# Kernel optimization log

Measured on AMD Instinct MI355X. Metric: run time of the kernel, lower is better.

Reference implementation:

```python
import jax, jax.numpy as jnp
import numpy as np

N_SUB, N_AGR, N_URB = 100000, 200000, 100000
E_SS, E_AS, E_US = 1_600_000, 400_000, 200_000
D_SUB, D_HRU, H, OUT, L = 128, 32, 128, 16, 3


def setup_inputs() -> dict:
    key = jax.random.key(0)
    ks = jax.random.split(key, 20)
    s = 0.05
    inp = {
        "x_sub": jax.random.normal(ks[0], (N_SUB, D_SUB), jnp.float32),
        "x_agr": jax.random.normal(ks[1], (N_AGR, D_HRU), jnp.float32),
        "x_urb": jax.random.normal(ks[2], (N_URB, D_HRU), jnp.float32),
        "ss_src": jax.random.randint(ks[3], (E_SS,), 0, N_SUB, jnp.int32),
        "ss_dst": jax.random.randint(ks[4], (E_SS,), 0, N_SUB, jnp.int32),
        "as_src": jax.random.randint(ks[5], (E_AS,), 0, N_AGR, jnp.int32),
        "as_dst": jax.random.randint(ks[6], (E_AS,), 0, N_SUB, jnp.int32),
        "us_src": jax.random.randint(ks[7], (E_US,), 0, N_URB, jnp.int32),
        "us_dst": jax.random.randint(ks[8], (E_US,), 0, N_SUB, jnp.int32),
        # Stacked per-layer SAGEConv params (in_sub == hidden, so uniform shapes).
        # lin_l (neighbor path, has bias) and lin_r (root path, no bias).
        "Wl_ss": jax.random.normal(ks[9], (L, H, H), jnp.float32) * s,
        "bl_ss": jnp.zeros((L, H), jnp.float32),
        "Wr_ss": jax.random.normal(ks[10], (L, H, H), jnp.float32) * s,
        "Wl_as": jax.random.normal(ks[11], (L, D_HRU, H), jnp.float32) * s,
        "bl_as": jnp.zeros((L, H), jnp.float32),
        "Wr_as": jax.random.normal(ks[12], (L, H, H), jnp.float32) * s,
        "Wl_us": jax.random.normal(ks[13], (L, D_HRU, H), jnp.float32) * s,
        "bl_us": jnp.zeros((L, H), jnp.float32),
        "Wr_us": jax.random.normal(ks[14], (L, H, H), jnp.float32) * s,
        "Wf": jax.random.normal(ks[15], (H, OUT), jnp.float32) * s,
        "bf": jnp.zeros((OUT,), jnp.float32),
    }
    return inp


def reference(x_sub, x_agr, x_urb, ss_src, ss_dst, as_src, as_dst, us_src,
              us_dst, Wl_ss, bl_ss, Wr_ss, Wl_as, bl_as, Wr_as, Wl_us, bl_us,
              Wr_us, Wf, bf):
    # Degree of each sub node under sub->sub edges (for mean aggr, layers>0).
    deg = jax.ops.segment_sum(jnp.ones((E_SS,), x_sub.dtype), ss_dst,
                              num_segments=N_SUB)
    deg = jnp.maximum(deg, 1.0)[:, None]  # [N_SUB,1]

    h = x_sub
    for i in range(L):
        # sub -> sub: gather + scatter-add (sum at layer 0, mean afterwards)
        agg_ss = jax.ops.segment_sum(h[ss_src], ss_dst, num_segments=N_SUB)
        if i > 0:
            agg_ss = agg_ss / deg  # PyG default aggr='mean' for layers > 0
        # hru_agr -> sub and hru_urb -> sub: sum aggregation (sage_aggr='sum')
        agg_as = jax.ops.segment_sum(x_agr[as_src], as_dst, num_segments=N_SUB)
        agg_us = jax.ops.segment_sum(x_urb[us_src], us_dst, num_segments=N_SUB)
        # SAGEConv: lin_l(aggr msgs) + lin_r(x_dst); HeteroConv aggr='sum'.
        out = (agg_ss @ Wl_ss[i] + bl_ss[i] + h @ Wr_ss[i]
               + agg_as @ Wl_as[i] + bl_as[i] + h @ Wr_as[i]
               + agg_us @ Wl_us[i] + bl_us[i] + h @ Wr_us[i])
        h = jax.nn.relu(out)  # norms are Identity; dropout in eval mode
    logits = h @ Wf + bf
    return jax.nn.softmax(logits, axis=1)
```

## Files before the change

### kernel.cpp

```cpp
#include <hip/hip_runtime.h>
#include <hip/hip_bf16.h>

#define N_SUB 100000
#define N_AGR 200000
#define N_URB 100000
#define E_SS  1600000
#define E_AS  400000
#define E_US  200000
#define E_TOT 2200000
#define HID   128
#define DHRU  32
#define NOUT  16
#define NL    3
#define SCAN_T 12500

typedef unsigned short u16;
typedef unsigned int u32;
typedef long long i64;
typedef short bf16x8 __attribute__((ext_vector_type(8)));
typedef float f32x4 __attribute__((ext_vector_type(4)));

#define FIXS 4294967296.0f
#define FIXR 2.3283064365386963e-10f

static __device__ __forceinline__ u16 f2b(float f) {
    u32 x = __float_as_uint(f);
    u32 r = (x + 0x7fffu + ((x >> 16) & 1u)) >> 16;
    return (u16)r;
}
static __device__ __forceinline__ float blo(u32 u) { return __uint_as_float(u << 16); }
static __device__ __forceinline__ float bhi(u32 u) { return __uint_as_float(u & 0xffff0000u); }
static __device__ __forceinline__ i64 fx(float v) { return (i64)(v * FIXS); }


__global__ void hist3_kernel(const int* __restrict__ ss_dst, const int* __restrict__ as_dst,
                             const int* __restrict__ us_dst, int* __restrict__ deg_ss,
                             int* __restrict__ deg_as, int* __restrict__ deg_us) {
    int i = blockIdx.x * 256 + threadIdx.x;
    if (i < E_SS) atomicAdd(&deg_ss[ss_dst[i]], 1);
    else if (i < E_SS + E_AS) atomicAdd(&deg_as[as_dst[i - E_SS]], 1);
    else if (i < E_TOT) atomicAdd(&deg_us[us_dst[i - E_SS - E_AS]], 1);
}

__global__ void scan_p1(const int* __restrict__ deg, int* __restrict__ tsum) {
    int i = blockIdx.x * 256 + threadIdx.x;
    if (i >= 3 * SCAN_T) return;
    const int4* p = (const int4*)(deg + i * 8);
    int4 a = p[0], b = p[1];
    tsum[i] = a.x + a.y + a.z + a.w + b.x + b.y + b.z + b.w;
}

__global__ void scan_p2(int* __restrict__ tsum_all) {
    __shared__ int sh[256];
    int* tsum = tsum_all + blockIdx.x * SCAN_T;
    const int tid = threadIdx.x;
    const int start = tid * 49;
    const int end = min(start + 49, SCAN_T);
    int s = 0;
    for (int i = start; i < end; ++i) s += tsum[i];
    sh[tid] = s;
    __syncthreads();
    for (int o = 1; o < 256; o <<= 1) {
        int t = (tid >= o) ? sh[tid - o] : 0;
        __syncthreads();
        sh[tid] += t;
        __syncthreads();
    }
    int off = (tid > 0) ? sh[tid - 1] : 0;
    for (int i = start; i < end; ++i) {
        int v = tsum[i];
        tsum[i] = off;
        off += v;
    }
}

__global__ void scan_p3(int* __restrict__ degcur, const int* __restrict__ tsum,
                        int* __restrict__ ro_ss, int* __restrict__ ro_as,
                        int* __restrict__ ro_us, float* __restrict__ inv_deg) {
    int i = blockIdx.x * 256 + threadIdx.x;
    if (i >= 3 * SCAN_T) return;
    int seg = i / SCAN_T, li = i - seg * SCAN_T;
    int* ro = (seg == 0) ? ro_ss : (seg == 1) ? ro_as : ro_us;
    int off = tsum[i];
#pragma unroll
    for (int j = 0; j < 8; ++j) {
        int gidx = i * 8 + j;
        int idx = li * 8 + j;
        int d = degcur[gidx];
        ro[idx] = off;
        if (seg == 0) inv_deg[idx] = 1.0f / (float)(d > 1 ? d : 1);
        degcur[gidx] = off;
        off += d;
    }
    if (li == SCAN_T - 1) ro[N_SUB] = off;
}

__global__ void fill3_kernel(const int* __restrict__ ss_src, const int* __restrict__ ss_dst,
                             const int* __restrict__ as_src, const int* __restrict__ as_dst,
                             const int* __restrict__ us_src, const int* __restrict__ us_dst,
                             int* __restrict__ cur_ss, int* __restrict__ cur_as,
                             int* __restrict__ cur_us, int* __restrict__ csr_ss,
                             int* __restrict__ csr_as, int* __restrict__ csr_us) {
    int i = blockIdx.x * 256 + threadIdx.x;
    const int* src; const int* dst; int* cur; int* csr; int e;
    if (i < E_SS)               { src = ss_src; dst = ss_dst; cur = cur_ss; csr = csr_ss; e = i; }
    else if (i < E_SS + E_AS)   { src = as_src; dst = as_dst; cur = cur_as; csr = csr_as; e = i - E_SS; }
    else if (i < E_TOT)         { src = us_src; dst = us_dst; cur = cur_us; csr = csr_us; e = i - E_SS - E_AS; }
    else return;
    int p = atomicAdd(&cur[dst[e]], 1);
    csr[p] = src[e];
}

__global__ __launch_bounds__(256)
void agg2_gather(const float* __restrict__ x_agr, const float* __restrict__ x_urb,
                 const int* __restrict__ ro_as, const int* __restrict__ csr_as,
                 const int* __restrict__ ro_us, const int* __restrict__ csr_us,
                 u16* __restrict__ agg2b, int n) {
    int node = blockIdx.x * 4 + (threadIdx.x >> 6);
    int lane = threadIdx.x & 63;
    if (node >= n) return;
    const bool is_us = lane >= 32;
    const int col = lane & 31;
    const int* ro = is_us ? ro_us : ro_as;
    const int* csr = is_us ? csr_us : csr_as;
    const float* x = is_us ? x_urb : x_agr;
    int beg = ro[node], end = ro[node + 1];
    i64 acc = 0;
    for (int p = beg; p < end; ++p) {
        acc += fx(x[(size_t)csr[p] * 32 + col]);
    }
    agg2b[(size_t)node * 64 + lane] = f2b((float)acc * FIXR);
}

__global__ void add3_kernel(const float* __restrict__ a, const float* __restrict__ b,
                            const float* __restrict__ c, float* __restrict__ o, int n) {
    int i = blockIdx.x * 256 + threadIdx.x;
    if (i < n) o[i] = a[i] + b[i] + c[i];
}

__global__ void build_bp(const float* __restrict__ Wl_ss, const float* __restrict__ Wr_ss,
                         const float* __restrict__ Wr_as, const float* __restrict__ Wr_us,
                         const float* __restrict__ Wl_as, const float* __restrict__ Wl_us,
                         u16* __restrict__ Bp) {
    int b = blockIdx.x;
    int lane = threadIdx.x;
    int lay = b / 80, rem = b % 80, s = rem / 8, c = rem % 8;
    int col = c * 16 + (lane & 15);
    u16* o = Bp + (size_t)(((lay * 80) + s * 8 + c) * 64 + lane) * 8;
#pragma unroll
    for (int j = 0; j < 8; ++j) {
        int k = s * 32 + (lane >> 4) * 8 + j;
        float v;
        if (k < 128) {
            v = Wl_ss[((size_t)lay * 128 + k) * 128 + col];
        } else if (k < 256) {
            size_t idx = ((size_t)lay * 128 + (k - 128)) * 128 + col;
            v = Wr_ss[idx] + Wr_as[idx] + Wr_us[idx];
        } else if (k < 288) {
            v = Wl_as[((size_t)lay * 32 + (k - 256)) * 128 + col];
        } else {
            v = Wl_us[((size_t)lay * 32 + (k - 288)) * 128 + col];
        }
        o[j] = f2b(v);
    }
}

__global__ void cvt_f32_bf16(const float* __restrict__ in, u16* __restrict__ o, int n4) {
    int i = blockIdx.x * 256 + threadIdx.x;
    if (i >= n4) return;
    float4 v = ((const float4*)in)[i];
    ushort4 u;
    u.x = f2b(v.x); u.y = f2b(v.y); u.z = f2b(v.z); u.w = f2b(v.w);
    ((ushort4*)o)[i] = u;
}

__global__ __launch_bounds__(256)
void agg_ss_bf16(const u16* __restrict__ h, const int* __restrict__ ro,
                 const int* __restrict__ csr, const float* __restrict__ inv_deg,
                 u16* __restrict__ out, int n, int use_mean) {
    int node = blockIdx.x * 4 + (threadIdx.x >> 6);
    if (node >= n) return;
    int lane = threadIdx.x & 63;
    int g = lane >> 4, t = lane & 15;
    int beg = ro[node], end = ro[node + 1];
    i64 acc[8] = {0, 0, 0, 0, 0, 0, 0, 0};
    int p = beg;
    for (; p + 3 < end; p += 4) {
        int s = csr[p + g];
        uint4 q = *(const uint4*)(h + (size_t)s * 128 + t * 8);
        acc[0] += fx(blo(q.x)); acc[1] += fx(bhi(q.x));
        acc[2] += fx(blo(q.y)); acc[3] += fx(bhi(q.y));
        acc[4] += fx(blo(q.z)); acc[5] += fx(bhi(q.z));
        acc[6] += fx(blo(q.w)); acc[7] += fx(bhi(q.w));
    }
    int rem = end - p;
    if (g < rem) {
        int s = csr[p + g];
        uint4 q = *(const uint4*)(h + (size_t)s * 128 + t * 8);
        acc[0] += fx(blo(q.x)); acc[1] += fx(bhi(q.x));
        acc[2] += fx(blo(q.y)); acc[3] += fx(bhi(q.y));
        acc[4] += fx(blo(q.z)); acc[5] += fx(bhi(q.z));
        acc[6] += fx(blo(q.w)); acc[7] += fx(bhi(q.w));
    }
#pragma unroll
    for (int j = 0; j < 8; ++j) {
        acc[j] += __shfl_xor(acc[j], 16, 64);
        acc[j] += __shfl_xor(acc[j], 32, 64);
    }
    if (g == 0) {
        float v[8];
        float iv = use_mean ? inv_deg[node] : 1.0f;
#pragma unroll
        for (int j = 0; j < 8; ++j) v[j] = (float)acc[j] * FIXR * iv;
        uint4 o;
        o.x = (u32)f2b(v[0]) | ((u32)f2b(v[1]) << 16);
        o.y = (u32)f2b(v[2]) | ((u32)f2b(v[3]) << 16);
        o.z = (u32)f2b(v[4]) | ((u32)f2b(v[5]) << 16);
        o.w = (u32)f2b(v[6]) | ((u32)f2b(v[7]) << 16);
        *(uint4*)(out + (size_t)node * 128 + t * 8) = o;
    }
}

__global__ __launch_bounds__(256)
void layer_gemm_mfma(const u16* __restrict__ agss, const u16* __restrict__ h,
                     const u16* __restrict__ agg2b, const u16* __restrict__ Bp,
                     const float* __restrict__ bsum, u16* __restrict__ out, int n) {
    __shared__ __align__(16) u16 tile[4][32][136];
    const int tid = threadIdx.x;
    const int w = tid >> 6, l = tid & 63;
    const int lr = l & 15, lq = l >> 4;
    const int rows0 = blockIdx.x * 128 + w * 32;

    f32x4 acc[2][8];
#pragma unroll
    for (int rf = 0; rf < 2; ++rf)
#pragma unroll
        for (int c = 0; c < 8; ++c) acc[rf][c] = (f32x4){0.f, 0.f, 0.f, 0.f};

    const bf16x8 zf = {0, 0, 0, 0, 0, 0, 0, 0};

#pragma unroll
    for (int s = 0; s < 10; ++s) {
        const u16* X;
        int ld, koff;
        if (s < 4)      { X = agss;  ld = 128; koff = s * 32 + lq * 8; }
        else if (s < 8) { X = h;     ld = 128; koff = (s - 4) * 32 + lq * 8; }
        else            { X = agg2b; ld = 64;  koff = (s - 8) * 32 + lq * 8; }
        bf16x8 a[2];
#pragma unroll
        for (int rf = 0; rf < 2; ++rf) {
            int row = rows0 + rf * 16 + lr;
            a[rf] = (row < n) ? *(const bf16x8*)(X + (size_t)row * ld + koff) : zf;
        }
        const u16* bp = Bp + ((size_t)(s * 8) * 64 + l) * 8;
#pragma unroll
        for (int c = 0; c < 8; ++c) {
            bf16x8 b = *(const bf16x8*)(bp + (size_t)c * 64 * 8);
            acc[0][c] = __builtin_amdgcn_mfma_f32_16x16x32_bf16(a[0], b, acc[0][c], 0, 0, 0);
            acc[1][c] = __builtin_amdgcn_mfma_f32_16x16x32_bf16(a[1], b, acc[1][c], 0, 0, 0);
        }
    }

    float bias[8];
#pragma unroll
    for (int c = 0; c < 8; ++c) bias[c] = bsum[c * 16 + lr];

#pragma unroll
    for (int rf = 0; rf < 2; ++rf)
#pragma unroll
        for (int c = 0; c < 8; ++c)
#pragma unroll
            for (int r = 0; r < 4; ++r) {
                float v = fmaxf(acc[rf][c][r] + bias[c], 0.f);
                tile[w][rf * 16 + lq * 4 + r][c * 16 + lr] = f2b(v);
            }

#pragma unroll
    for (int i = 0; i < 8; ++i) {
        int row = i * 4 + lq;
        int grow = rows0 + row;
        if (grow < n)
            *(bf16x8*)(out + (size_t)grow * 128 + lr * 8) =
                *(const bf16x8*)&tile[w][row][lr * 8];
    }
}

__global__ __launch_bounds__(256)
void final_kernel(const u32* __restrict__ h32, const float* __restrict__ Wf,
                  const float* __restrict__ bfv, float* __restrict__ out, int n) {
    __shared__ float wsh[HID * NOUT + NOUT];
    for (int i = threadIdx.x; i < HID * NOUT; i += 256) wsh[i] = Wf[i];
    if (threadIdx.x < NOUT) wsh[HID * NOUT + threadIdx.x] = bfv[threadIdx.x];
    __syncthreads();
    int t = blockIdx.x * 256 + threadIdx.x;
    int node = t >> 4, c = t & 15;
    if (node >= n) return;
    const u32* hr = h32 + (size_t)node * 64;
    float acc = wsh[HID * NOUT + c];
#pragma unroll 4
    for (int k2 = 0; k2 < 64; ++k2) {
        u32 u = hr[k2];
        acc += blo(u) * wsh[(2 * k2) * NOUT + c] + bhi(u) * wsh[(2 * k2 + 1) * NOUT + c];
    }
    float m = acc;
#pragma unroll
    for (int o = 8; o >= 1; o >>= 1) m = fmaxf(m, __shfl_xor(m, o, 16));
    float e = expf(acc - m);
    float ssum = e;
#pragma unroll
    for (int o = 8; o >= 1; o >>= 1) ssum += __shfl_xor(ssum, o, 16);
    out[(size_t)node * NOUT + c] = e / ssum;
}

extern "C" void kernel_launch(void* const* d_in, const int* in_sizes, int n_in,
                              void* d_out, int out_size, void* d_ws, size_t ws_size,
                              hipStream_t stream) {
    const float* x_sub = (const float*)d_in[0];
    const float* x_agr = (const float*)d_in[1];
    const float* x_urb = (const float*)d_in[2];
    const int* ss_src = (const int*)d_in[3];
    const int* ss_dst = (const int*)d_in[4];
    const int* as_src = (const int*)d_in[5];
    const int* as_dst = (const int*)d_in[6];
    const int* us_src = (const int*)d_in[7];
    const int* us_dst = (const int*)d_in[8];
    const float* Wl_ss = (const float*)d_in[9];
    const float* bl_ss = (const float*)d_in[10];
    const float* Wr_ss = (const float*)d_in[11];
    const float* Wl_as = (const float*)d_in[12];
    const float* bl_as = (const float*)d_in[13];
    const float* Wr_as = (const float*)d_in[14];
    const float* Wl_us = (const float*)d_in[15];
    const float* bl_us = (const float*)d_in[16];
    const float* Wr_us = (const float*)d_in[17];
    const float* Wf = (const float*)d_in[18];
    const float* bfv = (const float*)d_in[19];
    float* out = (float*)d_out;

    char* ws = (char*)d_ws;
    u16* h0      = (u16*)(ws + 0);
    u16* hA      = (u16*)(ws + 25600000);
    u16* hB      = (u16*)(ws + 51200000);
    u16* agss    = (u16*)(ws + 76800000);
    u16* agg2b   = (u16*)(ws + 102400000);
    float* inv_deg = (float*)(ws + 115200000);
    int* ro_ss   = (int*)(ws + 115600000);
    int* ro_as   = (int*)(ws + 116000016);
    int* ro_us   = (int*)(ws + 116400032);
    int* deg_ss  = (int*)(ws + 116800048);
    int* deg_as  = (int*)(ws + 117200048);
    int* deg_us  = (int*)(ws + 117600048);
    int* csr_ss  = (int*)(ws + 118000048);
    int* csr_as  = (int*)(ws + 124400048);
    int* csr_us  = (int*)(ws + 126000048);
    int* tsum    = (int*)(ws + 126800048);
    u16* Bp      = (u16*)(ws + 126950048);
    float* b_sum = (float*)(ws + 127195808);

    hipMemsetAsync(deg_ss, 0, 3 * N_SUB * sizeof(int), stream);
    hist3_kernel<<<(E_TOT + 255) / 256, 256, 0, stream>>>(ss_dst, as_dst, us_dst,
                                                          deg_ss, deg_as, deg_us);
    scan_p1<<<(3 * SCAN_T + 255) / 256, 256, 0, stream>>>(deg_ss, tsum);
    scan_p2<<<3, 256, 0, stream>>>(tsum);
    scan_p3<<<(3 * SCAN_T + 255) / 256, 256, 0, stream>>>(deg_ss, tsum, ro_ss, ro_as,
                                                          ro_us, inv_deg);
    fill3_kernel<<<(E_TOT + 255) / 256, 256, 0, stream>>>(ss_src, ss_dst, as_src, as_dst,
                                                          us_src, us_dst, deg_ss, deg_as,
                                                          deg_us, csr_ss, csr_as, csr_us);

    agg2_gather<<<(N_SUB + 3) / 4, 256, 0, stream>>>(x_agr, x_urb, ro_as, csr_as,
                                                     ro_us, csr_us, agg2b, N_SUB);

    build_bp<<<240, 64, 0, stream>>>(Wl_ss, Wr_ss, Wr_as, Wr_us, Wl_as, Wl_us, Bp);
    add3_kernel<<<2, 256, 0, stream>>>(bl_ss, bl_as, bl_us, b_sum, NL * HID);

    cvt_f32_bf16<<<(N_SUB * HID / 4 + 255) / 256, 256, 0, stream>>>(x_sub, h0, N_SUB * HID / 4);

    const int agg_grid = (N_SUB + 3) / 4;
    const int gemm_grid = (N_SUB + 127) / 128;
    const size_t BPL = 40960;

    agg_ss_bf16<<<agg_grid, 256, 0, stream>>>(h0, ro_ss, csr_ss, inv_deg, agss, N_SUB, 0);
    layer_gemm_mfma<<<gemm_grid, 256, 0, stream>>>(agss, h0, agg2b, Bp + 0 * BPL,
                                                   b_sum + 0 * HID, hA, N_SUB);

    agg_ss_bf16<<<agg_grid, 256, 0, stream>>>(hA, ro_ss, csr_ss, inv_deg, agss, N_SUB, 1);
    layer_gemm_mfma<<<gemm_grid, 256, 0, stream>>>(agss, hA, agg2b, Bp + 1 * BPL,
                                                   b_sum + 1 * HID, hB, N_SUB);

    agg_ss_bf16<<<agg_grid, 256, 0, stream>>>(hB, ro_ss, csr_ss, inv_deg, agss, N_SUB, 1);
    layer_gemm_mfma<<<gemm_grid, 256, 0, stream>>>(agss, hB, agg2b, Bp + 2 * BPL,
                                                   b_sum + 2 * HID, hA, N_SUB);

    final_kernel<<<(N_SUB * NOUT + 255) / 256, 256, 0, stream>>>((const u32*)hA, Wf, bfv,
                                                                 out, N_SUB);
}
```

Baseline: 799.7 us.

## Build CSR via two-pass bucketed scatter and unroll ss aggregation gather

Replaces the single-pass CSR fill, which did one global atomic per edge on per-node counters scattered across memory, with a two-pass scheme. Edges are first scattered into 64-node buckets with packed (local dst, src) words, then each bucket is placed into CSR order using shared-memory atomics. This aims to cut contention and random global atomics, but adds an extra pass over staging memory that reuses the agss buffer region. The sub-sub aggregation loop is also unrolled to issue two neighbor row loads per iteration for more memory-level parallelism.

New measurement: 931.5 us. 1.16x slower.

```diff
diff --git a/kernel.cpp b/kernel.cpp
--- a/kernel.cpp
+++ b/kernel.cpp
@@ -13,6 +13,7 @@
 #define NOUT  16
 #define NL    3
 #define SCAN_T 12500
+#define NB    1563
 
 typedef unsigned short u16;
 typedef unsigned int u32;
@@ -95,20 +96,54 @@
     if (li == SCAN_T - 1) ro[N_SUB] = off;
 }
 
-__global__ void fill3_kernel(const int* __restrict__ ss_src, const int* __restrict__ ss_dst,
-                             const int* __restrict__ as_src, const int* __restrict__ as_dst,
-                             const int* __restrict__ us_src, const int* __restrict__ us_dst,
-                             int* __restrict__ cur_ss, int* __restrict__ cur_as,
-                             int* __restrict__ cur_us, int* __restrict__ csr_ss,
-                             int* __restrict__ csr_as, int* __restrict__ csr_us) {
-    int i = blockIdx.x * 256 + threadIdx.x;
-    const int* src; const int* dst; int* cur; int* csr; int e;
-    if (i < E_SS)               { src = ss_src; dst = ss_dst; cur = cur_ss; csr = csr_ss; e = i; }
-    else if (i < E_SS + E_AS)   { src = as_src; dst = as_dst; cur = cur_as; csr = csr_as; e = i - E_SS; }
-    else if (i < E_TOT)         { src = us_src; dst = us_dst; cur = cur_us; csr = csr_us; e = i - E_SS - E_AS; }
+__global__ void binit_kernel(const int* __restrict__ ro_ss, const int* __restrict__ ro_as,
+                             const int* __restrict__ ro_us, int* __restrict__ bcur) {
+    int i = blockIdx.x * 256 + threadIdx.x;
+    if (i >= 3 * NB) return;
+    int t = i / NB, k = i - t * NB;
+    const int* ro = (t == 0) ? ro_ss : (t == 1) ? ro_as : ro_us;
+    bcur[i] = ro[k * 64];
+}
+
+__global__ void bucket_scatter(const int* __restrict__ ss_src, const int* __restrict__ ss_dst,
+                               const int* __restrict__ as_src, const int* __restrict__ as_dst,
+                               const int* __restrict__ us_src, const int* __restrict__ us_dst,
+                               int* __restrict__ bcur, u32* __restrict__ stg_ss,
+                               u32* __restrict__ stg_as, u32* __restrict__ stg_us) {
+    int i = blockIdx.x * 256 + threadIdx.x;
+    const int* src; const int* dst; u32* stg; int e, t;
+    if (i < E_SS)               { src = ss_src; dst = ss_dst; stg = stg_ss; e = i; t = 0; }
+    else if (i < E_SS + E_AS)   { src = as_src; dst = as_dst; stg = stg_as; e = i - E_SS; t = 1; }
+    else if (i < E_TOT)         { src = us_src; dst = us_dst; stg = stg_us; e = i - E_SS - E_AS; t = 2; }
     else return;
-    int p = atomicAdd(&cur[dst[e]], 1);
-    csr[p] = src[e];
+    int d = dst[e];
+    int pos = atomicAdd(&bcur[t * NB + (d >> 6)], 1);
+    stg[pos] = ((u32)(d & 63) << 18) | (u32)src[e];
+}
+
+__global__ __launch_bounds__(256)
+void bucket_fill(const int* __restrict__ ro_ss, const int* __restrict__ ro_as,
+                 const int* __restrict__ ro_us, const u32* __restrict__ stg_ss,
+                 const u32* __restrict__ stg_as, const u32* __restrict__ stg_us,
+                 int* __restrict__ csr_ss, int* __restrict__ csr_as,
+                 int* __restrict__ csr_us) {
+    __shared__ int cur[64];
+    int b = blockIdx.x;
+    int t = b / NB, k = b - t * NB;
+    const int* ro = (t == 0) ? ro_ss : (t == 1) ? ro_as : ro_us;
+    const u32* stg = (t == 0) ? stg_ss : (t == 1) ? stg_as : stg_us;
+    int* csr = (t == 0) ? csr_ss : (t == 1) ? csr_as : csr_us;
+    int base = k * 64;
+    int nodes = min(64, N_SUB - base);
+    if (threadIdx.x < nodes) cur[threadIdx.x] = ro[base + threadIdx.x];
+    int start = ro[base];
+    int end = ro[base + nodes];
+    __syncthreads();
+    for (int pos = start + threadIdx.x; pos < end; pos += 256) {
+        u32 u = stg[pos];
+        int p = atomicAdd(&cur[u >> 18], 1);
+        csr[p] = (int)(u & 0x3FFFFu);
+    }
 }
 
 __global__ __launch_bounds__(256)
@@ -185,13 +220,24 @@
     int beg = ro[node], end = ro[node + 1];
     i64 acc[8] = {0, 0, 0, 0, 0, 0, 0, 0};
     int p = beg;
-    for (; p + 3 < end; p += 4) {
+    for (; p + 7 < end; p += 8) {
+        int s0 = csr[p + g];
+        int s1 = csr[p + 4 + g];
+        uint4 q0 = *(const uint4*)(h + (size_t)s0 * 128 + t * 8);
+        uint4 q1 = *(const uint4*)(h + (size_t)s1 * 128 + t * 8);
+        acc[0] += fx(blo(q0.x)) + fx(blo(q1.x)); acc[1] += fx(bhi(q0.x)) + fx(bhi(q1.x));
+        acc[2] += fx(blo(q0.y)) + fx(blo(q1.y)); acc[3] += fx(bhi(q0.y)) + fx(bhi(q1.y));
+        acc[4] += fx(blo(q0.z)) + fx(blo(q1.z)); acc[5] += fx(bhi(q0.z)) + fx(bhi(q1.z));
+        acc[6] += fx(blo(q0.w)) + fx(blo(q1.w)); acc[7] += fx(bhi(q0.w)) + fx(bhi(q1.w));
+    }
+    if (p + 3 < end) {
         int s = csr[p + g];
         uint4 q = *(const uint4*)(h + (size_t)s * 128 + t * 8);
         acc[0] += fx(blo(q.x)); acc[1] += fx(bhi(q.x));
         acc[2] += fx(blo(q.y)); acc[3] += fx(bhi(q.y));
         acc[4] += fx(blo(q.z)); acc[5] += fx(bhi(q.z));
         acc[6] += fx(blo(q.w)); acc[7] += fx(bhi(q.w));
+        p += 4;
     }
     int rem = end - p;
     if (g < rem) {
@@ -342,6 +388,9 @@
     u16* hA      = (u16*)(ws + 25600000);
     u16* hB      = (u16*)(ws + 51200000);
     u16* agss    = (u16*)(ws + 76800000);
+    u32* stg_ss  = (u32*)(ws + 76800000);
+    u32* stg_as  = (u32*)(ws + 83200000);
+    u32* stg_us  = (u32*)(ws + 84800000);
     u16* agg2b   = (u16*)(ws + 102400000);
     float* inv_deg = (float*)(ws + 115200000);
     int* ro_ss   = (int*)(ws + 115600000);
@@ -356,6 +405,7 @@
     int* tsum    = (int*)(ws + 126800048);
     u16* Bp      = (u16*)(ws + 126950048);
     float* b_sum = (float*)(ws + 127195808);
+    int* bcur    = (int*)(ws + 127197344);
 
     hipMemsetAsync(deg_ss, 0, 3 * N_SUB * sizeof(int), stream);
     hist3_kernel<<<(E_TOT + 255) / 256, 256, 0, stream>>>(ss_dst, as_dst, us_dst,
@@ -364,9 +414,12 @@
     scan_p2<<<3, 256, 0, stream>>>(tsum);
     scan_p3<<<(3 * SCAN_T + 255) / 256, 256, 0, stream>>>(deg_ss, tsum, ro_ss, ro_as,
                                                           ro_us, inv_deg);
-    fill3_kernel<<<(E_TOT + 255) / 256, 256, 0, stream>>>(ss_src, ss_dst, as_src, as_dst,
-                                                          us_src, us_dst, deg_ss, deg_as,
-                                                          deg_us, csr_ss, csr_as, csr_us);
+    binit_kernel<<<(3 * NB + 255) / 256, 256, 0, stream>>>(ro_ss, ro_as, ro_us, bcur);
+    bucket_scatter<<<(E_TOT + 255) / 256, 256, 0, stream>>>(ss_src, ss_dst, as_src, as_dst,
+                                                            us_src, us_dst, bcur,
+                                                            stg_ss, stg_as, stg_us);
+    bucket_fill<<<3 * NB, 256, 0, stream>>>(ro_ss, ro_as, ro_us, stg_ss, stg_as, stg_us,
+                                            csr_ss, csr_as, csr_us);
 
     agg2_gather<<<(N_SUB + 3) / 4, 256, 0, stream>>>(x_agr, x_urb, ro_as, csr_as,
                                                      ro_us, csr_us, agg2b, N_SUB);
```

## Slice sub-sub neighbor gather by source range for cache locality

Applied to the files above, without the earlier changes.

Rewrites the sub->sub aggregation so each wave processes neighbors in 8 passes over source-id ranges, and each lane reads one u32 (2 bf16 values) per neighbor instead of 4 edges in parallel with uint4 loads. The goal is for all in-flight waves to touch roughly the same slice of h at once, so gathers hit L2/MALL more often. The cost is 8x rescanning of the CSR index list, branchy per-edge checks, and less memory-level parallelism per wave. It also makes the CSR fill use nontemporal stores.

Result: slower. 2.273 ms (+184.2%).

```diff
diff --git a/kernel.cpp b/kernel.cpp
--- a/kernel.cpp
+++ b/kernel.cpp
@@ -13,6 +13,8 @@
 #define NOUT  16
 #define NL    3
 #define SCAN_T 12500
+#define NSLICE 8
+#define SLICE_W 12500
 
 typedef unsigned short u16;
 typedef unsigned int u32;
@@ -108,7 +110,7 @@
     else if (i < E_TOT)         { src = us_src; dst = us_dst; cur = cur_us; csr = csr_us; e = i - E_SS - E_AS; }
     else return;
     int p = atomicAdd(&cur[dst[e]], 1);
-    csr[p] = src[e];
+    __builtin_nontemporal_store(src[e], &csr[p]);
 }
 
 __global__ __launch_bounds__(256)
@@ -175,50 +177,30 @@
 }
 
 __global__ __launch_bounds__(256)
-void agg_ss_bf16(const u16* __restrict__ h, const int* __restrict__ ro,
+void agg_ss_bf16(const u32* __restrict__ h32, const int* __restrict__ ro,
                  const int* __restrict__ csr, const float* __restrict__ inv_deg,
-                 u16* __restrict__ out, int n, int use_mean) {
+                 u32* __restrict__ out32, int n, int use_mean) {
     int node = blockIdx.x * 4 + (threadIdx.x >> 6);
     if (node >= n) return;
     int lane = threadIdx.x & 63;
-    int g = lane >> 4, t = lane & 15;
     int beg = ro[node], end = ro[node + 1];
-    i64 acc[8] = {0, 0, 0, 0, 0, 0, 0, 0};
-    int p = beg;
-    for (; p + 3 < end; p += 4) {
-        int s = csr[p + g];
-        uint4 q = *(const uint4*)(h + (size_t)s * 128 + t * 8);
-        acc[0] += fx(blo(q.x)); acc[1] += fx(bhi(q.x));
-        acc[2] += fx(blo(q.y)); acc[3] += fx(bhi(q.y));
-        acc[4] += fx(blo(q.z)); acc[5] += fx(bhi(q.z));
-        acc[6] += fx(blo(q.w)); acc[7] += fx(bhi(q.w));
-    }
-    int rem = end - p;
-    if (g < rem) {
-        int s = csr[p + g];
-        uint4 q = *(const uint4*)(h + (size_t)s * 128 + t * 8);
-        acc[0] += fx(blo(q.x)); acc[1] += fx(bhi(q.x));
-        acc[2] += fx(blo(q.y)); acc[3] += fx(bhi(q.y));
-        acc[4] += fx(blo(q.z)); acc[5] += fx(bhi(q.z));
-        acc[6] += fx(blo(q.w)); acc[7] += fx(bhi(q.w));
-    }
-#pragma unroll
-    for (int j = 0; j < 8; ++j) {
-        acc[j] += __shfl_xor(acc[j], 16, 64);
-        acc[j] += __shfl_xor(acc[j], 32, 64);
-    }
-    if (g == 0) {
-        float v[8];
-        float iv = use_mean ? inv_deg[node] : 1.0f;
-#pragma unroll
-        for (int j = 0; j < 8; ++j) v[j] = (float)acc[j] * FIXR * iv;
-        uint4 o;
-        o.x = (u32)f2b(v[0]) | ((u32)f2b(v[1]) << 16);
-        o.y = (u32)f2b(v[2]) | ((u32)f2b(v[3]) << 16);
-        o.z = (u32)f2b(v[4]) | ((u32)f2b(v[5]) << 16);
-        o.w = (u32)f2b(v[6]) | ((u32)f2b(v[7]) << 16);
-        *(uint4*)(out + (size_t)node * 128 + t * 8) = o;
-    }
+    i64 a0 = 0, a1 = 0;
+#pragma unroll 1
+    for (int r = 0; r < NSLICE; ++r) {
+        int lo = r * SLICE_W, hi = lo + SLICE_W;
+        for (int p = beg; p < end; ++p) {
+            int s = csr[p];
+            if (s >= lo && s < hi) {
+                u32 u = h32[(size_t)s * 64 + lane];
+                a0 += fx(blo(u));
+                a1 += fx(bhi(u));
+            }
+        }
+    }
+    float iv = use_mean ? inv_deg[node] : 1.0f;
+    float v0 = (float)a0 * FIXR * iv;
+    float v1 = (float)a1 * FIXR * iv;
+    out32[(size_t)node * 64 + lane] = (u32)f2b(v0) | ((u32)f2b(v1) << 16);
 }
 
 __global__ __launch_bounds__(256)
@@ -380,15 +362,18 @@
     const int gemm_grid = (N_SUB + 127) / 128;
     const size_t BPL = 40960;
 
-    agg_ss_bf16<<<agg_grid, 256, 0, stream>>>(h0, ro_ss, csr_ss, inv_deg, agss, N_SUB, 0);
+    agg_ss_bf16<<<agg_grid, 256, 0, stream>>>((const u32*)h0, ro_ss, csr_ss, inv_deg,
+                                              (u32*)agss, N_SUB, 0);
     layer_gemm_mfma<<<gemm_grid, 256, 0, stream>>>(agss, h0, agg2b, Bp + 0 * BPL,
                                                    b_sum + 0 * HID, hA, N_SUB);
 
-    agg_ss_bf16<<<agg_grid, 256, 0, stream>>>(hA, ro_ss, csr_ss, inv_deg, agss, N_SUB, 1);
+    agg_ss_bf16<<<agg_grid, 256, 0, stream>>>((const u32*)hA, ro_ss, csr_ss, inv_deg,
+                                              (u32*)agss, N_SUB, 1);
     layer_gemm_mfma<<<gemm_grid, 256, 0, stream>>>(agss, hA, agg2b, Bp + 1 * BPL,
                                                    b_sum + 1 * HID, hB, N_SUB);
 
-    agg_ss_bf16<<<agg_grid, 256, 0, stream>>>(hB, ro_ss, csr_ss, inv_deg, agss, N_SUB, 1);
+    agg_ss_bf16<<<agg_grid, 256, 0, stream>>>((const u32*)hB, ro_ss, csr_ss, inv_deg,
+                                              (u32*)agss, N_SUB, 1);
     layer_gemm_mfma<<<gemm_grid, 256, 0, stream>>>(agss, hB, agg2b, Bp + 2 * BPL,
                                                    b_sum + 2 * HID, hA, N_SUB);
 
```
